# Kernel tuning notes

Measured on AMD Instinct MI355X. Metric: run time of the kernel, lower is better.

## Reference

```python
import jax, jax.numpy as jnp
import numpy as np

H = 512
B, T = 16, 600
LN_EPS = 1e-5


def _lstm_dir(x, w_ih, w_hh, b, reverse):
    # x: [B,T,In], w_ih: [4H,In], w_hh: [4H,H], b: [4H] (b_ih+b_hh combined)
    if reverse:
        x = jnp.flip(x, axis=1)
    xp = jnp.einsum('bti,gi->btg', x, w_ih) + b  # [B,T,4H] gate preactivations from input
    h0 = jnp.zeros((x.shape[0], w_hh.shape[1]), x.dtype)
    c0 = jnp.zeros_like(h0)

    def step(carry, g_t):
        h, c = carry
        g = g_t + h @ w_hh.T
        i, f, gg, o = jnp.split(g, 4, axis=-1)  # torch gate order: i,f,g,o
        i = jax.nn.sigmoid(i)
        f = jax.nn.sigmoid(f)
        gg = jnp.tanh(gg)
        o = jax.nn.sigmoid(o)
        c = f * c + i * gg
        h = o * jnp.tanh(c)
        return (h, c), h

    _, hs = jax.lax.scan(step, (h0, c0), jnp.swapaxes(xp, 0, 1))
    hs = jnp.swapaxes(hs, 0, 1)  # [B,T,H]
    if reverse:
        hs = jnp.flip(hs, axis=1)
    return hs


def setup_inputs() -> dict:
    key = jax.random.key(0)
    ks = jax.random.split(key, 20)
    s = 1.0 / np.sqrt(H)
    u = lambda k, shape: jax.random.uniform(k, shape, jnp.float32, -s, s)
    inp = {'x': jax.random.normal(ks[0], (B, H, T), jnp.float32)}
    # layer 0: input H; layer 1: input 2H (bidirectional concat)
    inp['w_ih_l0f'] = u(ks[1], (4 * H, H));     inp['w_hh_l0f'] = u(ks[2], (4 * H, H));  inp['b_l0f'] = u(ks[3], (4 * H,))
    inp['w_ih_l0b'] = u(ks[4], (4 * H, H));     inp['w_hh_l0b'] = u(ks[5], (4 * H, H));  inp['b_l0b'] = u(ks[6], (4 * H,))
    inp['w_ih_l1f'] = u(ks[7], (4 * H, 2 * H)); inp['w_hh_l1f'] = u(ks[8], (4 * H, H));  inp['b_l1f'] = u(ks[9], (4 * H,))
    inp['w_ih_l1b'] = u(ks[10], (4 * H, 2 * H)); inp['w_hh_l1b'] = u(ks[11], (4 * H, H)); inp['b_l1b'] = u(ks[12], (4 * H,))
    inp['fc_w'] = u(ks[13], (H, 2 * H))
    inp['fc_b'] = u(ks[14], (H,))
    inp['ln_w'] = jnp.ones((H,), jnp.float32)
    inp['ln_b'] = jnp.zeros((H,), jnp.float32)
    return inp


def reference(x, w_ih_l0f, w_hh_l0f, b_l0f, w_ih_l0b, w_hh_l0b, b_l0b,
              w_ih_l1f, w_hh_l1f, b_l1f, w_ih_l1b, w_hh_l1b, b_l1b,
              fc_w, fc_b, ln_w, ln_b):
    xt = jnp.transpose(x, (0, 2, 1))  # [B,T,H]
    # layer 0 (bi)
    h0f = _lstm_dir(xt, w_ih_l0f, w_hh_l0f, b_l0f, False)
    h0b = _lstm_dir(xt, w_ih_l0b, w_hh_l0b, b_l0b, True)
    h0 = jnp.concatenate([h0f, h0b], axis=-1)  # [B,T,2H]
    # layer 1 (bi)
    h1f = _lstm_dir(h0, w_ih_l1f, w_hh_l1f, b_l1f, False)
    h1b = _lstm_dir(h0, w_ih_l1b, w_hh_l1b, b_l1b, True)
    h1 = jnp.concatenate([h1f, h1b], axis=-1)  # [B,T,2H]
    # fc -> layernorm -> relu
    out = jnp.einsum('btk,hk->bth', h1, fc_w) + fc_b
    mu = jnp.mean(out, axis=-1, keepdims=True)
    var = jnp.mean(jnp.square(out - mu), axis=-1, keepdims=True)
    out = (out - mu) * jax.lax.rsqrt(var + LN_EPS) * ln_w + ln_b
    return jax.nn.relu(out)
```

## Files before the change

### kernel.cpp

```cpp
#include <hip/hip_runtime.h>
#include <hip/hip_bf16.h>

#define HDIM 512
#define BATCH 16
#define TSEQ 600
#define NROW (BATCH*TSEQ)

typedef unsigned short u16;
typedef unsigned long long u64;
typedef __attribute__((ext_vector_type(8))) short short8;
typedef __attribute__((ext_vector_type(4))) float f32x4;
typedef __attribute__((ext_vector_type(4))) int i32x4;

__device__ __forceinline__ u16 f2b(float f){
  unsigned x; __builtin_memcpy(&x, &f, 4);
  x += 0x7fffu + ((x >> 16) & 1u);
  return (u16)(x >> 16);
}
__device__ __forceinline__ float b2f(u16 u){
  unsigned x = ((unsigned)u) << 16; float f; __builtin_memcpy(&f, &x, 4); return f;
}

#define LOG2E 1.44269504f
__device__ __forceinline__ float fsig(float x){
  return __builtin_amdgcn_rcpf(1.f + __builtin_amdgcn_exp2f(-x*LOG2E));
}
__device__ __forceinline__ float ftanh(float x){
  return 2.f*__builtin_amdgcn_rcpf(1.f + __builtin_amdgcn_exp2f(-2.f*LOG2E*x)) - 1.f;
}

__global__ void cvt_kernel(const float* __restrict__ in, u16* __restrict__ out, int n4){
  int i = blockIdx.x*blockDim.x + threadIdx.x;
  if (i < n4){
    float4 v = ((const float4*)in)[i];
    ushort4 u; u.x=f2b(v.x); u.y=f2b(v.y); u.z=f2b(v.z); u.w=f2b(v.w);
    ((ushort4*)out)[i] = u;
  }
}

__global__ void maxabs4_kernel(const float* __restrict__ a, const float* __restrict__ b,
                               const float* __restrict__ c, const float* __restrict__ d,
                               unsigned* __restrict__ outmax, int n){
  const float* p = (blockIdx.y==0)?a:(blockIdx.y==1)?b:(blockIdx.y==2)?c:d;
  float m = 0.f;
  for (int i = blockIdx.x*blockDim.x + threadIdx.x; i < n; i += gridDim.x*blockDim.x)
    m = fmaxf(m, fabsf(p[i]));
  for (int off=32; off>0; off>>=1) m = fmaxf(m, __shfl_down(m, off));
  if ((threadIdx.x & 63) == 0) atomicMax(outmax + blockIdx.y, __float_as_uint(m));
}

__global__ void quantw4_kernel(const float* __restrict__ a, const float* __restrict__ b,
                               const float* __restrict__ c, const float* __restrict__ d,
                               const unsigned* __restrict__ maxu,
                               signed char* __restrict__ oa, signed char* __restrict__ ob,
                               signed char* __restrict__ oc, signed char* __restrict__ od, int n4){
  int i = blockIdx.x*blockDim.x + threadIdx.x;
  if (i >= n4) return;
  const float* p = (blockIdx.y==0)?a:(blockIdx.y==1)?b:(blockIdx.y==2)?c:d;
  signed char* o = (blockIdx.y==0)?oa:(blockIdx.y==1)?ob:(blockIdx.y==2)?oc:od;
  float s = 127.f / fmaxf(__uint_as_float(maxu[blockIdx.y]), 1e-20f);
  float4 v = ((const float4*)p)[i];
  unsigned x0 = (unsigned)((int)rintf(v.x*s) & 255);
  unsigned x1 = (unsigned)((int)rintf(v.y*s) & 255);
  unsigned x2 = (unsigned)((int)rintf(v.z*s) & 255);
  unsigned x3 = (unsigned)((int)rintf(v.w*s) & 255);
  ((unsigned*)o)[i] = x0 | (x1<<8) | (x2<<16) | (x3<<24);
}

__global__ __launch_bounds__(256) void transpose_kernel(const float* __restrict__ x, u16* __restrict__ xt){
  __shared__ float tile[32][33];
  int t0 = blockIdx.x*32, h0 = blockIdx.y*32, b = blockIdx.z;
  int li = threadIdx.x & 31, lj = threadIdx.x >> 5;
  for (int j=lj; j<32; j+=8){
    int t = t0 + li;
    tile[j][li] = (t < TSEQ) ? x[((size_t)b*HDIM + h0 + j)*TSEQ + t] : 0.f;
  }
  __syncthreads();
  for (int j=lj; j<32; j+=8){
    int t = t0 + j;
    if (t < TSEQ) xt[((size_t)b*TSEQ + t)*HDIM + h0 + li] = f2b(tile[li][j]);
  }
}

template<typename OT>
__global__ __launch_bounds__(256) void gemm_bt(const u16* __restrict__ A, const u16* __restrict__ B,
    const float* __restrict__ bias, OT* __restrict__ C, int M, int N, int K)
{
  __shared__ u16 As[128][40];
  __shared__ u16 Bs[128][40];
  const int m0 = blockIdx.x*128, n0 = blockIdx.y*128;
  const int tid = threadIdx.x, lane = tid & 63;
  const int wr = ((tid>>6)&1)*64, wc = ((tid>>6)>>1)*64;
  const int srow = tid>>2, scol = (tid&3)*8;
  f32x4 acc[4][4] = {};
  for (int k0=0; k0<K; k0+=32){
    uint4 a0 = *(const uint4*)(A + (size_t)(m0+srow)*K    + k0 + scol);
    uint4 a1 = *(const uint4*)(A + (size_t)(m0+srow+64)*K + k0 + scol);
    uint4 b0 = *(const uint4*)(B + (size_t)(n0+srow)*K    + k0 + scol);
    uint4 b1 = *(const uint4*)(B + (size_t)(n0+srow+64)*K + k0 + scol);
    __syncthreads();
    *(uint4*)&As[srow][scol]    = a0;
    *(uint4*)&As[srow+64][scol] = a1;
    *(uint4*)&Bs[srow][scol]    = b0;
    *(uint4*)&Bs[srow+64][scol] = b1;
    __syncthreads();
    short8 af[4], bfr[4];
#pragma unroll
    for (int i=0;i<4;i++) af[i]  = *(const short8*)&As[wr + i*16 + (lane&15)][(lane>>4)*8];
#pragma unroll
    for (int i=0;i<4;i++) bfr[i] = *(const short8*)&Bs[wc + i*16 + (lane&15)][(lane>>4)*8];
#pragma unroll
    for (int i=0;i<4;i++)
#pragma unroll
      for (int j=0;j<4;j++)
        acc[i][j] = __builtin_amdgcn_mfma_f32_16x16x32_bf16(af[i], bfr[j], acc[i][j], 0,0,0);
  }
#pragma unroll
  for (int i=0;i<4;i++)
#pragma unroll
    for (int j=0;j<4;j++){
      int row = m0 + wr + i*16 + (lane>>4)*4;
      int col = n0 + wc + j*16 + (lane&15);
      float bv = bias ? bias[col] : 0.f;
#pragma unroll
      for (int r=0;r<4;r++){
        float v = acc[i][j][r] + bv;
        if (sizeof(OT) == 2) C[(size_t)(row+r)*N + col] = (OT)f2b(v);
        else                 C[(size_t)(row+r)*N + col] = (OT)v;
      }
    }
}

__global__ __launch_bounds__(512, 1) void lstm_rec11(
    const u16* __restrict__ xp_f, const u16* __restrict__ xp_b,
    const signed char* __restrict__ w8_f, const signed char* __restrict__ w8_b,
    const unsigned* __restrict__ maxu,
    u16* __restrict__ h_out,
    u64* __restrict__ dpl,
    unsigned* __restrict__ tags)
{
  const int bi = blockIdx.x, rem = bi & 7;
  if (rem > 1) return;
  const int dir = rem, wid = bi >> 3;
  const int tid = threadIdx.x, lane = tid & 63, w = tid >> 6;
  const int l15 = lane & 15, lq = lane >> 4;
  const int P = wid*128 + w*16;

  const u16* xp = dir ? xp_b : xp_f;
  const signed char* w8 = dir ? w8_b : w8_f;
  const float mx = __uint_as_float(maxu[dir]);
  const float sA = mx / (127.f*127.f);

  __shared__ __align__(16) signed char hL[2][16][528];

  i32x4 wf[4][8];
#pragma unroll
  for (int g=0; g<4; ++g)
#pragma unroll
    for (int kk=0; kk<8; ++kk)
      wf[g][kk] = *(const i32x4*)(w8 + (size_t)(g*512 + P + l15)*512 + kk*64 + lq*16);

  u64* pl = dpl + (size_t)dir*(2*2048);
  const int mychunk = l15*128 + (P >> 2) + lq;
  const int cb = tid >> 5, cp16 = tid & 31;
  const int cP = (cp16 >> 3)*128 + (cp16 & 7)*16;
  const int coff = cb*128 + (cP >> 2);

  float c[4] = {0.f,0.f,0.f,0.f};
  const int t0 = dir ? (TSEQ-1) : 0, ts = dir ? -1 : 1;

  for (int s=0; s<TSEQ; ++s){
    const int t = t0 + s*ts;
    const int par = s & 1;

    ushort4 xq[4];
    {
      const u16* px = xp + ((size_t)(l15*TSEQ + t))*2048 + P + lq*4;
#pragma unroll
      for (int g=0; g<4; ++g) xq[g] = *(const ushort4*)(px + g*512);
    }

    {
      const u64* q = pl + (size_t)par*2048 + coff;
      u64 v[4];
#pragma unroll
      for (int i=0;i<4;i++)
        v[i] = __hip_atomic_load(q+i, __ATOMIC_RELAXED, __HIP_MEMORY_SCOPE_AGENT);
      {
        const unsigned* tp = tags + ((dir*2 + par)*32 + cp16)*4;
        while ((int)__hip_atomic_load(tp, __ATOMIC_RELAXED, __HIP_MEMORY_SCOPE_AGENT) < s) {}
      }
      for (;;){
        bool ok = true;
#pragma unroll
        for (int i=0;i<4;i++) ok &= ((unsigned)(v[i] >> 32) == (unsigned)s);
        if (ok) break;
#pragma unroll
        for (int i=0;i<4;i++)
          if ((unsigned)(v[i] >> 32) != (unsigned)s)
            v[i] = __hip_atomic_load(q+i, __ATOMIC_RELAXED, __HIP_MEMORY_SCOPE_AGENT);
      }
      u64 lo = (u64)(unsigned)v[0] | ((u64)(unsigned)v[1] << 32);
      u64 hi = (u64)(unsigned)v[2] | ((u64)(unsigned)v[3] << 32);
      *(u64*)&hL[par][cb][cP]     = lo;
      *(u64*)&hL[par][cb][cP + 8] = hi;
    }
    __syncthreads();

    i32x4 acc[4] = {};
#pragma unroll
    for (int kk=0; kk<8; ++kk){
      i32x4 b1 = *(const i32x4*)(&hL[par][l15][0] + kk*64 + lq*16);
#pragma unroll
      for (int g=0; g<4; ++g)
        acc[g] = __builtin_amdgcn_mfma_i32_16x16x64_i8(wf[g][kk], b1, acc[g], 0, 0, 0);
    }

    unsigned pk1 = 0; float hhv[4];
#pragma unroll
    for (int r=0; r<4; ++r){
      float pre[4];
#pragma unroll
      for (int g=0; g<4; ++g)
        pre[g] = b2f(((const u16*)&xq[g])[r]) + sA*(float)acc[g][r];
      float iv = fsig(pre[0]);
      float fv = fsig(pre[1]);
      float gv = ftanh(pre[2]);
      float ov = fsig(pre[3]);
      float cc = fv*c[r] + iv*gv; c[r] = cc;
      float hh = ov*ftanh(cc);
      hhv[r] = hh;
      int d1i = (int)rintf(hh*127.f);
      pk1 |= (unsigned)(d1i & 255) << (8*r);
    }
    if (s < TSEQ-1){
      u64 chunk = ((u64)(unsigned)(s+1) << 32) | (u64)pk1;
      __hip_atomic_store(pl + (size_t)(par^1)*2048 + mychunk, chunk,
                         __ATOMIC_RELAXED, __HIP_MEMORY_SCOPE_AGENT);
      if (lane == 0){
        unsigned* tg = tags + ((dir*2 + (par^1))*32 + wid*8 + w)*4;
        __hip_atomic_store(tg, (unsigned)(s+1), __ATOMIC_RELAXED, __HIP_MEMORY_SCOPE_AGENT);
      }
    }
    ushort4 hu;
#pragma unroll
    for (int r=0; r<4; ++r) ((u16*)&hu)[r] = f2b(hhv[r]);
    *(ushort4*)(h_out + ((size_t)(l15*TSEQ + t))*1024 + dir*512 + P + lq*4) = hu;
  }
}

__global__ __launch_bounds__(256) void ln_relu_kernel(const float* __restrict__ in,
    const float* __restrict__ gw, const float* __restrict__ gb, float* __restrict__ out)
{
  __shared__ float rs[4], rss[4];
  const int row = blockIdx.x;
  const float* p = in + (size_t)row*HDIM;
  float v0 = p[threadIdx.x], v1 = p[threadIdx.x + 256];
  float s = v0 + v1, ss = v0*v0 + v1*v1;
  for (int off=32; off>0; off>>=1){
    s  += __shfl_down(s, off);
    ss += __shfl_down(ss, off);
  }
  if ((threadIdx.x & 63) == 0){ rs[threadIdx.x>>6] = s; rss[threadIdx.x>>6] = ss; }
  __syncthreads();
  float st  = rs[0]+rs[1]+rs[2]+rs[3];
  float sst = rss[0]+rss[1]+rss[2]+rss[3];
  float mu  = st * (1.f/HDIM);
  float var = sst * (1.f/HDIM) - mu*mu;
  float rstd = rsqrtf(var + 1e-5f);
  int c0 = threadIdx.x, c1 = threadIdx.x + 256;
  float y0 = (v0 - mu)*rstd*gw[c0] + gb[c0];
  float y1 = (v1 - mu)*rstd*gw[c1] + gb[c1];
  out[(size_t)row*HDIM + c0] = fmaxf(y0, 0.f);
  out[(size_t)row*HDIM + c1] = fmaxf(y1, 0.f);
}

extern "C" void kernel_launch(void* const* d_in, const int* in_sizes, int n_in,
                              void* d_out, int out_size, void* d_ws, size_t ws_size,
                              hipStream_t stream)
{
  const float* x        = (const float*)d_in[0];
  const float* wih_l0f  = (const float*)d_in[1];
  const float* whh_l0f  = (const float*)d_in[2];
  const float* b_l0f    = (const float*)d_in[3];
  const float* wih_l0b  = (const float*)d_in[4];
  const float* whh_l0b  = (const float*)d_in[5];
  const float* b_l0b    = (const float*)d_in[6];
  const float* wih_l1f  = (const float*)d_in[7];
  const float* whh_l1f  = (const float*)d_in[8];
  const float* b_l1f    = (const float*)d_in[9];
  const float* wih_l1b  = (const float*)d_in[10];
  const float* whh_l1b  = (const float*)d_in[11];
  const float* b_l1b    = (const float*)d_in[12];
  const float* fc_w     = (const float*)d_in[13];
  const float* fc_b     = (const float*)d_in[14];
  const float* ln_w     = (const float*)d_in[15];
  const float* ln_b     = (const float*)d_in[16];
  float* outp = (float*)d_out;

  char* base = (char*)d_ws;
  size_t off = 0;
  auto alloc = [&](size_t bytes)->char*{ char* p = base + off; off += (bytes + 255) & ~(size_t)255; return p; };

  unsigned* maxu = (unsigned*)alloc(256);
  u64* dpl0 = (u64*)alloc((size_t)2*2*2048*8);
  u64* dpl1 = (u64*)alloc((size_t)2*2*2048*8);
  unsigned* tags0 = (unsigned*)alloc((size_t)2*2*32*16);
  unsigned* tags1 = (unsigned*)alloc((size_t)2*2*32*16);
  size_t zero_bytes = off;
  signed char* w8_l0f = (signed char*)alloc((size_t)2048*512);
  signed char* w8_l0b = (signed char*)alloc((size_t)2048*512);
  signed char* w8_l1f = (signed char*)alloc((size_t)2048*512);
  signed char* w8_l1b = (signed char*)alloc((size_t)2048*512);
  u16* xt     = (u16*)alloc((size_t)NROW*512*2);
  u16* wb_l0f = (u16*)alloc((size_t)2048*512*2);
  u16* wb_l0b = (u16*)alloc((size_t)2048*512*2);
  u16* wb_l1f = (u16*)alloc((size_t)2048*1024*2);
  u16* wb_l1b = (u16*)alloc((size_t)2048*1024*2);
  u16* wb_fc  = (u16*)alloc((size_t)512*1024*2);
  u16* h0     = (u16*)alloc((size_t)NROW*1024*2);
  u16* h1     = (u16*)alloc((size_t)NROW*1024*2);
  u16* xpf    = (u16*)alloc((size_t)NROW*2048*2);
  u16* xpb    = (u16*)alloc((size_t)NROW*2048*2);
  float* fco  = (float*)alloc((size_t)NROW*512*4);
  (void)ws_size; (void)in_sizes; (void)n_in; (void)out_size;

  hipMemsetAsync(d_ws, 0, zero_bytes, stream);

  auto cvt = [&](const float* in, u16* out, int n){
    int n4 = n/4;
    cvt_kernel<<<dim3((n4+255)/256), 256, 0, stream>>>(in, out, n4);
  };
  cvt(wih_l0f, wb_l0f, 2048*512);
  cvt(wih_l0b, wb_l0b, 2048*512);
  cvt(wih_l1f, wb_l1f, 2048*1024);
  cvt(wih_l1b, wb_l1b, 2048*1024);
  cvt(fc_w,    wb_fc,  512*1024);

  maxabs4_kernel<<<dim3(64,4), 256, 0, stream>>>(whh_l0f, whh_l0b, whh_l1f, whh_l1b, maxu, 2048*512);
  quantw4_kernel<<<dim3((2048*512/4+255)/256,4), 256, 0, stream>>>(
      whh_l0f, whh_l0b, whh_l1f, whh_l1b, maxu, w8_l0f, w8_l0b, w8_l1f, w8_l1b, 2048*512/4);

  transpose_kernel<<<dim3(19,16,16), 256, 0, stream>>>(x, xt);

  gemm_bt<u16><<<dim3(75,16), 256, 0, stream>>>(xt, wb_l0f, b_l0f, xpf, NROW, 2048, 512);
  gemm_bt<u16><<<dim3(75,16), 256, 0, stream>>>(xt, wb_l0b, b_l0b, xpb, NROW, 2048, 512);
  lstm_rec11<<<dim3(32), 512, 0, stream>>>(xpf, xpb, w8_l0f, w8_l0b, maxu+0, h0, dpl0, tags0);

  gemm_bt<u16><<<dim3(75,16), 256, 0, stream>>>(h0, wb_l1f, b_l1f, xpf, NROW, 2048, 1024);
  gemm_bt<u16><<<dim3(75,16), 256, 0, stream>>>(h0, wb_l1b, b_l1b, xpb, NROW, 2048, 1024);
  lstm_rec11<<<dim3(32), 512, 0, stream>>>(xpf, xpb, w8_l1f, w8_l1b, maxu+2, h1, dpl1, tags1);

  gemm_bt<float><<<dim3(75,4), 256, 0, stream>>>(h1, wb_fc, fc_b, fco, NROW, 512, 1024);
  ln_relu_kernel<<<dim3(NROW), 256, 0, stream>>>(fco, ln_w, ln_b, outp);
}
```

Before: 4.627 ms.

## Compute local h slice before waiting on remote blocks in LSTM recurrence

Each block now writes its own quantized h slice straight into shared memory and reorders the K loop so its local two K-chunks come first. Those MFMAs run before the block polls the cross-block flags, so part of the matvec overlaps the wait for other blocks. Only foreign chunks are fetched through the global mailbox. In exchange it adds an extra __syncthreads per step and a zeroing pass over shared memory at kernel start.

```diff
diff --git a/kernel.cpp b/kernel.cpp
--- a/kernel.cpp
+++ b/kernel.cpp
@@ -131,7 +131,7 @@
     }
 }
 
-__global__ __launch_bounds__(512, 1) void lstm_rec11(
+__global__ __launch_bounds__(512, 1) void lstm_rec12(
     const u16* __restrict__ xp_f, const u16* __restrict__ xp_b,
     const signed char* __restrict__ w8_f, const signed char* __restrict__ w8_b,
     const unsigned* __restrict__ maxu,
@@ -157,14 +157,21 @@
 #pragma unroll
   for (int g=0; g<4; ++g)
 #pragma unroll
-    for (int kk=0; kk<8; ++kk)
-      wf[g][kk] = *(const i32x4*)(w8 + (size_t)(g*512 + P + l15)*512 + kk*64 + lq*16);
+    for (int j=0; j<8; ++j){
+      const int kkp = (wid*2 + j) & 7;
+      wf[g][j] = *(const i32x4*)(w8 + (size_t)(g*512 + P + l15)*512 + kkp*64 + lq*16);
+    }
 
   u64* pl = dpl + (size_t)dir*(2*2048);
   const int mychunk = l15*128 + (P >> 2) + lq;
   const int cb = tid >> 5, cp16 = tid & 31;
-  const int cP = (cp16 >> 3)*128 + (cp16 & 7)*16;
+  const int cwid = cp16 >> 3;
+  const int cP = cwid*128 + (cp16 & 7)*16;
   const int coff = cb*128 + (cP >> 2);
+  const bool foreign = (cwid != wid);
+
+  for (int i = tid; i < 2*16*528/4; i += 512) ((unsigned*)hL)[i] = 0u;
+  __syncthreads();
 
   float c[4] = {0.f,0.f,0.f,0.f};
   const int t0 = dir ? (TSEQ-1) : 0, ts = dir ? -1 : 1;
@@ -180,16 +187,24 @@
       for (int g=0; g<4; ++g) xq[g] = *(const ushort4*)(px + g*512);
     }
 
-    {
+    i32x4 acc[4] = {};
+#pragma unroll
+    for (int j=0; j<2; ++j){
+      const int kkp = (wid*2 + j) & 7;
+      i32x4 b1 = *(const i32x4*)(&hL[par][l15][0] + kkp*64 + lq*16);
+#pragma unroll
+      for (int g=0; g<4; ++g)
+        acc[g] = __builtin_amdgcn_mfma_i32_16x16x64_i8(wf[g][j], b1, acc[g], 0, 0, 0);
+    }
+
+    if (foreign){
+      const unsigned* tp = tags + ((dir*2 + par)*32 + cp16)*4;
+      while ((int)__hip_atomic_load(tp, __ATOMIC_RELAXED, __HIP_MEMORY_SCOPE_AGENT) < s) {}
       const u64* q = pl + (size_t)par*2048 + coff;
       u64 v[4];
 #pragma unroll
       for (int i=0;i<4;i++)
         v[i] = __hip_atomic_load(q+i, __ATOMIC_RELAXED, __HIP_MEMORY_SCOPE_AGENT);
-      {
-        const unsigned* tp = tags + ((dir*2 + par)*32 + cp16)*4;
-        while ((int)__hip_atomic_load(tp, __ATOMIC_RELAXED, __HIP_MEMORY_SCOPE_AGENT) < s) {}
-      }
       for (;;){
         bool ok = true;
 #pragma unroll
@@ -207,13 +222,13 @@
     }
     __syncthreads();
 
-    i32x4 acc[4] = {};
-#pragma unroll
-    for (int kk=0; kk<8; ++kk){
-      i32x4 b1 = *(const i32x4*)(&hL[par][l15][0] + kk*64 + lq*16);
+#pragma unroll
+    for (int j=2; j<8; ++j){
+      const int kkp = (wid*2 + j) & 7;
+      i32x4 b1 = *(const i32x4*)(&hL[par][l15][0] + kkp*64 + lq*16);
 #pragma unroll
       for (int g=0; g<4; ++g)
-        acc[g] = __builtin_amdgcn_mfma_i32_16x16x64_i8(wf[g][kk], b1, acc[g], 0, 0, 0);
+        acc[g] = __builtin_amdgcn_mfma_i32_16x16x64_i8(wf[g][j], b1, acc[g], 0, 0, 0);
     }
 
     unsigned pk1 = 0; float hhv[4];
@@ -242,10 +257,12 @@
         __hip_atomic_store(tg, (unsigned)(s+1), __ATOMIC_RELAXED, __HIP_MEMORY_SCOPE_AGENT);
       }
     }
+    *(unsigned*)&hL[par^1][l15][P + lq*4] = pk1;
     ushort4 hu;
 #pragma unroll
     for (int r=0; r<4; ++r) ((u16*)&hu)[r] = f2b(hhv[r]);
     *(ushort4*)(h_out + ((size_t)(l15*TSEQ + t))*1024 + dir*512 + P + lq*4) = hu;
+    __syncthreads();
   }
 }
 
@@ -345,11 +362,11 @@
 
   gemm_bt<u16><<<dim3(75,16), 256, 0, stream>>>(xt, wb_l0f, b_l0f, xpf, NROW, 2048, 512);
   gemm_bt<u16><<<dim3(75,16), 256, 0, stream>>>(xt, wb_l0b, b_l0b, xpb, NROW, 2048, 512);
-  lstm_rec11<<<dim3(32), 512, 0, stream>>>(xpf, xpb, w8_l0f, w8_l0b, maxu+0, h0, dpl0, tags0);
+  lstm_rec12<<<dim3(32), 512, 0, stream>>>(xpf, xpb, w8_l0f, w8_l0b, maxu+0, h0, dpl0, tags0);
 
   gemm_bt<u16><<<dim3(75,16), 256, 0, stream>>>(h0, wb_l1f, b_l1f, xpf, NROW, 2048, 1024);
   gemm_bt<u16><<<dim3(75,16), 256, 0, stream>>>(h0, wb_l1b, b_l1b, xpb, NROW, 2048, 1024);
-  lstm_rec11<<<dim3(32), 512, 0, stream>>>(xpf, xpb, w8_l1f, w8_l1b, maxu+2, h1, dpl1, tags1);
+  lstm_rec12<<<dim3(32), 512, 0, stream>>>(xpf, xpb, w8_l1f, w8_l1b, maxu+2, h1, dpl1, tags1);
 
   gemm_bt<float><<<dim3(75,4), 256, 0, stream>>>(h1, wb_fc, fc_b, fco, NROW, 512, 1024);
   ln_relu_kernel<<<dim3(NROW), 256, 0, stream>>>(fco, ln_w, ln_b, outp);
```

Result: faster. 4.001 ms (-13.5%).
